# Kernel optimization log

Measured on AMD Instinct MI355X. Metric: run time of the kernel, lower is better.

Reference implementation:

```python
import jax, jax.numpy as jnp
import numpy as np

INPLANES = 768
HIDDEN = 64
NUM_EXPERTS = 6
TOP_K = 2


def setup_inputs() -> dict:
    key = jax.random.key(0)
    ks = jax.random.split(key, 7)
    B, C, D = 64, 320, INPLANES
    x = jax.random.normal(ks[0], (B, C, D), dtype=jnp.float32)
    xi = jax.random.normal(ks[1], (B, C, D), dtype=jnp.float32)
    # gating network: per-token logits over experts
    w_gate = jax.random.normal(ks[2], (D, NUM_EXPERTS), dtype=jnp.float32) / np.sqrt(D)
    # LoRA-style experts: down-projection D -> HIDDEN per expert
    expert_w = jax.random.normal(ks[3], (NUM_EXPERTS, D, HIDDEN), dtype=jnp.float32) / np.sqrt(D)
    expert_b = jnp.zeros((NUM_EXPERTS, HIDDEN), dtype=jnp.float32)
    # reprojection ffn1_1: Linear(HIDDEN, INPLANES), torch convention W:[out,in]
    ffn1_w = jax.random.normal(ks[4], (D, HIDDEN), dtype=jnp.float32) / np.sqrt(HIDDEN)
    ffn1_b = jnp.zeros((D,), dtype=jnp.float32)
    return {"x": x, "xi": xi, "w_gate": w_gate, "expert_w": expert_w,
            "expert_b": expert_b, "ffn1_w": ffn1_w, "ffn1_b": ffn1_b}


def _cv_squared(v):
    eps = 1e-10
    return jnp.var(v) / (jnp.mean(v) ** 2 + eps)


def reference(x, xi, w_gate, expert_w, expert_b, ffn1_w, ffn1_b):
    B, C, D = x.shape
    nz = C // 5
    # slice template (z) and search (x) token streams from both modalities
    z0, x0 = x[:, :nz, :], x[:, nz:, :]
    z1, x1 = xi[:, :nz, :], xi[:, nz:, :]
    # MoE_lora: fuse the two modalities and route tokens (z tokens first, then x)
    inp = jnp.concatenate([z0 + z1, x0 + x1], axis=1)        # [B, C, D]
    tok = inp.reshape(-1, D)                                  # [N, D], N = B*C
    N = tok.shape[0]
    # noisy-top-k gating (clean/eval path): top-2 experts, softmax over kept logits
    logits = tok @ w_gate                                     # [N, E]
    top_vals, top_idx = jax.lax.top_k(logits, TOP_K)          # [N, k]
    top_gates = jax.nn.softmax(top_vals, axis=-1)             # [N, k]
    gates = jnp.zeros_like(logits).at[jnp.arange(N)[:, None], top_idx].add(top_gates)
    # expert LoRA down-projections, combined by sparse gates (dense-equivalent math)
    h = jnp.einsum('nd,edh->enh', tok, expert_w) + expert_b[:, None, :]  # [E, N, H]
    y = jnp.einsum('ne,enh->nh', gates, h)                    # [N, H]
    y = y.reshape(B, C, HIDDEN)
    z_moe, x_moe = y[:, :nz, :], y[:, nz:, :]
    # load-balancing loss: cv^2 of importance + cv^2 of load
    importance = gates.sum(axis=0)
    load = (gates > 0).astype(jnp.float32).sum(axis=0)
    loss = _cv_squared(importance) + _cv_squared(load)
    # ffn1_1 reprojection back to inplanes
    x_prompted = x_moe @ ffn1_w.T + ffn1_b                    # [B, 4C/5, D]
    z_prompted = z_moe @ ffn1_w.T + ffn1_b                    # [B, C/5, D]
    return (x_prompted, z_prompted, loss, logits)
```

## Files before the change

kernel.cpp:

```cpp
#include <hip/hip_runtime.h>

typedef __attribute__((ext_vector_type(8))) short short8;
typedef __attribute__((ext_vector_type(4))) short short4v;
typedef __attribute__((ext_vector_type(4))) float f32x4;

#define VM(n) asm volatile("s_waitcnt vmcnt(" #n ")" ::: "memory")
#define LGKM0 asm volatile("s_waitcnt lgkmcnt(0)" ::: "memory")

namespace {

constexpr int DIN  = 768;
constexpr int HID  = 64;
constexpr int NEXP = 6;
constexpr int CDIM  = 320;
constexpr int NZ    = 64;
constexpr int NTOK  = 20480;

constexpr long long XP_OFF   = 0;
constexpr long long ZP_OFF   = 12582912LL;
constexpr long long LOSS_OFF = 15728640LL;
constexpr long long LG_OFF   = 15728641LL;

__device__ inline unsigned short f2bf(float f) {
  union { float f; unsigned u; } v{f};
  return (unsigned short)((v.u + 0x7FFFu + ((v.u >> 16) & 1u)) >> 16);
}
__device__ inline float b2f(unsigned short s) {
  union { unsigned u; float f; } v{(unsigned)s << 16};
  return v.f;
}
__device__ inline void gload16(const void* g, void* l) {
  __builtin_amdgcn_global_load_lds(
      (const __attribute__((address_space(1))) unsigned*)g,
      (__attribute__((address_space(3))) unsigned*)l, 16, 0, 0);
}
__device__ inline int row_base(int n) {
  int bb = n / CDIM, c = n - bb * CDIM;
  return (c < NZ) ? (int)(ZP_OFF + (long long)(bb * NZ + c) * DIN)
                  : (int)(XP_OFF + (long long)(bb * (CDIM - NZ) + (c - NZ)) * DIN);
}

__global__ __launch_bounds__(512) void pre_kernel(
    const float* __restrict__ x, const float* __restrict__ xi,
    const float* __restrict__ wg, const float* __restrict__ ew,
    const float* __restrict__ fw,
    float* __restrict__ out, float4* __restrict__ rec,
    unsigned short* __restrict__ ewb_t, unsigned short* __restrict__ fwb)
{
  int b = blockIdx.x, tid = threadIdx.x;
  __shared__ __align__(16) char sbuf[67584];
  if (b < 72) {
    float (*t_lds)[65] = (float(*)[65])sbuf;
    int e = b / 12, kc = (b % 12) * 64;
    const float* src = ew + (size_t)e * DIN * HID + (size_t)kc * HID;
    #pragma unroll
    for (int it = 0; it < 8; ++it) {
      int f = it * 512 + tid; int ky = f >> 6, h = f & 63;
      t_lds[h][ky] = src[ky * 64 + h];
    }
    __syncthreads();
    unsigned short* dst = ewb_t + (size_t)e * DIN * HID + kc;
    #pragma unroll
    for (int it = 0; it < 8; ++it) {
      int f = it * 512 + tid; int h = f >> 6, ky = f & 63;
      dst[(size_t)h * DIN + ky] = f2bf(t_lds[h][ky]);
    }
    return;
  }
  if (b < 84) {
    int base = (b - 72) * 4096;
    #pragma unroll
    for (int it = 0; it < 8; ++it) {
      int idx = base + it * 512 + tid;
      fwb[idx] = f2bf(fw[idx]);
    }
    return;
  }
  char* xl = sbuf;
  char* il = sbuf + 24576;
  const float* wgl = (const float*)(sbuf + 49152);
  int t0 = (b - 84) * 8;

  #pragma unroll
  for (int it = 0; it < 3; ++it) {
    int s = it * 512 + tid;
    gload16(x  + (size_t)t0 * DIN + s * 4, xl + s * 16);
    gload16(xi + (size_t)t0 * DIN + s * 4, il + s * 16);
  }
  #pragma unroll
  for (int it = 0; it < 3; ++it) {
    int s = it * 512 + tid;
    if (s < NEXP * DIN / 4) gload16(wg + s * 4, sbuf + 49152 + s * 16);
  }
  VM(0);
  __builtin_amdgcn_s_barrier();

  int lane = tid & 63, w = tid >> 6;
  int n = t0 + w;
  unsigned short* tk = (unsigned short*)out + (size_t)row_base(n) * 2;

  float lg[NEXP];
  #pragma unroll
  for (int e = 0; e < NEXP; ++e) lg[e] = 0.f;

  #pragma unroll
  for (int j = 0; j < 3; ++j) {
    int d = lane * 4 + 256 * j;
    float4 a = *(const float4*)(xl + w * 3072 + d * 4);
    float4 q = *(const float4*)(il + w * 3072 + d * 4);
    float tv0 = a.x + q.x, tv1 = a.y + q.y, tv2 = a.z + q.z, tv3 = a.w + q.w;
    short4v t4;
    t4[0] = (short)f2bf(tv0); t4[1] = (short)f2bf(tv1);
    t4[2] = (short)f2bf(tv2); t4[3] = (short)f2bf(tv3);
    *(short4v*)(tk + d) = t4;
    const float4* wq = (const float4*)(wgl + d * 6);
    float4 w0 = wq[0], w1 = wq[1], w2 = wq[2], w3 = wq[3], w4 = wq[4], w5 = wq[5];
    lg[0] += tv0 * w0.x; lg[1] += tv0 * w0.y; lg[2] += tv0 * w0.z;
    lg[3] += tv0 * w0.w; lg[4] += tv0 * w1.x; lg[5] += tv0 * w1.y;
    lg[0] += tv1 * w1.z; lg[1] += tv1 * w1.w; lg[2] += tv1 * w2.x;
    lg[3] += tv1 * w2.y; lg[4] += tv1 * w2.z; lg[5] += tv1 * w2.w;
    lg[0] += tv2 * w3.x; lg[1] += tv2 * w3.y; lg[2] += tv2 * w3.z;
    lg[3] += tv2 * w3.w; lg[4] += tv2 * w4.x; lg[5] += tv2 * w4.y;
    lg[0] += tv3 * w4.z; lg[1] += tv3 * w4.w; lg[2] += tv3 * w5.x;
    lg[3] += tv3 * w5.y; lg[4] += tv3 * w5.z; lg[5] += tv3 * w5.w;
  }
  #pragma unroll
  for (int e = 0; e < NEXP; ++e) {
    float v = lg[e];
    #pragma unroll
    for (int off = 32; off >= 1; off >>= 1) v += __shfl_xor(v, off, 64);
    lg[e] = v;
  }
  int e0 = 0; float v0 = lg[0];
  #pragma unroll
  for (int j = 1; j < NEXP; ++j) if (lg[j] > v0) { v0 = lg[j]; e0 = j; }
  int e1 = 0; float v1 = -3.4e38f;
  #pragma unroll
  for (int j = 0; j < NEXP; ++j) if (j != e0 && lg[j] > v1) { v1 = lg[j]; e1 = j; }
  float g0 = 1.f / (1.f + expf(v1 - v0));
  if (lane < NEXP) {
    float myv = lg[0];
    #pragma unroll
    for (int e = 1; e < NEXP; ++e) if (lane == e) myv = lg[e];
    out[LG_OFF + (size_t)n * NEXP + lane] = myv;
  }
  if (lane == 0) rec[n] = make_float4((float)e0, (float)e1, g0, 1.f - g0);
}

__global__ __launch_bounds__(512) void moe_kernel(
    const unsigned short* __restrict__ ewb_t, const float* __restrict__ eb,
    const unsigned short* __restrict__ fwb, const float* __restrict__ fb,
    const float4* __restrict__ rec, float* __restrict__ out)
{
  __shared__ __align__(16) char smem[74752];
  __shared__ int rb[64];
  __shared__ float simp[8][NEXP], sld[8][NEXP];

  int tid = threadIdx.x, lane = tid & 63, wid = tid >> 6;
  int qw = lane >> 4, l15 = lane & 15;
  int wm = wid >> 2, wn = wid & 3;

  if (blockIdx.x == 320) {
    float imp[NEXP], ld[NEXP];
    #pragma unroll
    for (int e = 0; e < NEXP; ++e) { imp[e] = 0.f; ld[e] = 0.f; }
    for (int n = tid; n < NTOK; n += 512) {
      float4 r = rec[n];
      int e0 = (int)r.x, e1 = (int)r.y;
      #pragma unroll
      for (int e = 0; e < NEXP; ++e) {
        imp[e] += (e == e0 ? r.z : 0.f) + (e == e1 ? r.w : 0.f);
        ld[e]  += (e == e0 ? 1.f : 0.f) + (e == e1 ? 1.f : 0.f);
      }
    }
    #pragma unroll
    for (int e = 0; e < NEXP; ++e) {
      float a = imp[e], bq = ld[e];
      #pragma unroll
      for (int off = 32; off >= 1; off >>= 1) {
        a += __shfl_xor(a, off, 64);
        bq += __shfl_xor(bq, off, 64);
      }
      imp[e] = a; ld[e] = bq;
    }
    if (lane == 0) {
      #pragma unroll
      for (int e = 0; e < NEXP; ++e) { simp[wid][e] = imp[e]; sld[wid][e] = ld[e]; }
    }
    __syncthreads();
    if (tid == 0) {
      float It[NEXP], Lt[NEXP], mi = 0.f, ml = 0.f;
      #pragma unroll
      for (int e = 0; e < NEXP; ++e) {
        It[e] = 0.f; Lt[e] = 0.f;
        #pragma unroll
        for (int w = 0; w < 8; ++w) { It[e] += simp[w][e]; Lt[e] += sld[w][e]; }
        mi += It[e]; ml += Lt[e];
      }
      mi /= NEXP; ml /= NEXP;
      float vi = 0.f, vl = 0.f;
      #pragma unroll
      for (int e = 0; e < NEXP; ++e) {
        vi += (It[e] - mi) * (It[e] - mi);
        vl += (Lt[e] - ml) * (Lt[e] - ml);
      }
      vi /= NEXP; vl /= NEXP;
      out[LOSS_OFF] = vi / (mi * mi + 1e-10f) + vl / (ml * ml + 1e-10f);
    }
    return;
  }

  int t0 = blockIdx.x * 64;
  const unsigned short* tokb = (const unsigned short*)out;

  size_t b_src[3]; int b_dst[3];
  #pragma unroll
  for (int it = 0; it < 3; ++it) {
    int F = it * 512 + tid, r = F >> 2, s = F & 3;
    b_src[it] = (size_t)r * DIN + ((s ^ (r & 3) ^ ((r & 4) >> 1)) << 3);
    b_dst[it] = (it * 512 + wid * 64) * 16;
  }
  int ar = tid >> 2, as = tid & 3;
  size_t a_src = (size_t)row_base(t0 + ar) * 2 +
                 ((as ^ (ar & 3) ^ ((ar & 4) >> 1)) << 3);
  int a_dst = (wid * 64) * 16;

  if (tid < 64) rb[tid] = row_base(t0 + tid);

  #pragma unroll
  for (int it = 0; it < 3; ++it)
    gload16(ewb_t + b_src[it], smem + 8192 + b_dst[it]);
  if (tid < 256) gload16(tokb + a_src, smem + a_dst);

  f32x4 acc[2][6];
  #pragma unroll
  for (int m = 0; m < 2; ++m)
    #pragma unroll
    for (int n = 0; n < 6; ++n) acc[m][n] = (f32x4){0.f, 0.f, 0.f, 0.f};

  int aoff[2], boff[6];
  #pragma unroll
  for (int m = 0; m < 2; ++m) {
    int row = wm * 32 + m * 16 + l15;
    aoff[m] = row * 64 + ((qw ^ (row & 3) ^ ((row & 4) >> 1)) << 4);
  }
  #pragma unroll
  for (int n = 0; n < 6; ++n) {
    int row = wn * 96 + n * 16 + l15;
    boff[n] = row * 64 + ((qw ^ (row & 3) ^ ((row & 4) >> 1)) << 4);
  }

  for (int k = 0; k < 24; ++k) {
    const char* cA = smem + (k & 1) * 4096;
    const char* cB = smem + 8192 + (k & 1) * 24576;
    char* nA = (char*)smem + ((k + 1) & 1) * 4096;
    char* nB = (char*)smem + 8192 + ((k + 1) & 1) * 24576;
    if (k < 23) {
      #pragma unroll
      for (int it = 0; it < 3; ++it)
        gload16(ewb_t + b_src[it] + (k + 1) * 32, nB + b_dst[it]);
      if (tid < 256) gload16(tokb + a_src + (k + 1) * 32, nA + a_dst);
      if (wid < 4) VM(4); else VM(3);
    } else {
      VM(0);
    }
    __builtin_amdgcn_s_barrier();
    __builtin_amdgcn_sched_barrier(0);
    short8 af[2], bfv[6];
    #pragma unroll
    for (int m = 0; m < 2; ++m) af[m] = *(const short8*)(cA + aoff[m]);
    #pragma unroll
    for (int n = 0; n < 6; ++n) bfv[n] = *(const short8*)(cB + boff[n]);
    __builtin_amdgcn_s_setprio(1);
    #pragma unroll
    for (int m = 0; m < 2; ++m)
      #pragma unroll
      for (int n = 0; n < 6; ++n)
        acc[m][n] = __builtin_amdgcn_mfma_f32_16x16x32_bf16(af[m], bfv[n], acc[m][n], 0, 0, 0);
    __builtin_amdgcn_s_setprio(0);
    __builtin_amdgcn_sched_barrier(0);
    __builtin_amdgcn_s_barrier();
  }

  #pragma unroll
  for (int it = 0; it < 2; ++it) {
    int F = it * 512 + tid, r = F >> 3, s = F & 7;
    gload16(fwb + (size_t)r * HID + ((s ^ (r & 7)) << 3),
            smem + 58368 + (it * 512 + wid * 64) * 16);
  }

  unsigned short* hl = (unsigned short*)(smem + 8192);
  #pragma unroll
  for (int m = 0; m < 2; ++m)
    #pragma unroll
    for (int n = 0; n < 6; ++n)
      #pragma unroll
      for (int i = 0; i < 4; ++i) {
        int row = wm * 32 + m * 16 + qw * 4 + i;
        int col = wn * 96 + n * 16 + l15;
        hl[row * 392 + col] = f2bf(acc[m][n][i]);
      }
  LGKM0;
  __builtin_amdgcn_s_barrier();

  {
    int t = tid >> 3, j0 = (tid & 7) * 8;
    float4 rr = rec[t0 + t];
    int e0 = (int)rr.x, e1 = (int)rr.y;
    float g0 = rr.z, g1 = rr.w;
    short8 h0 = *(const short8*)(hl + t * 392 + e0 * 64 + j0);
    short8 h1 = *(const short8*)(hl + t * 392 + e1 * 64 + j0);
    const float4* ep0 = (const float4*)(eb + e0 * 64 + j0);
    const float4* ep1 = (const float4*)(eb + e1 * 64 + j0);
    float4 b0a = ep0[0], b0b = ep0[1], b1a = ep1[0], b1b = ep1[1];
    float be0[8] = {b0a.x, b0a.y, b0a.z, b0a.w, b0b.x, b0b.y, b0b.z, b0b.w};
    float be1[8] = {b1a.x, b1a.y, b1a.z, b1a.w, b1b.x, b1b.y, b1b.z, b1b.w};
    short8 ov;
    #pragma unroll
    for (int j = 0; j < 8; ++j) {
      float v = g0 * (b2f((unsigned short)h0[j]) + be0[j])
              + g1 * (b2f((unsigned short)h1[j]) + be1[j]);
      ov[j] = (short)f2bf(v);
    }
    *(short8*)(smem + t * 128 + ((((tid & 7)) ^ (t & 7)) << 4)) = ov;
  }
  LGKM0;
  __builtin_amdgcn_s_barrier();

  for (int c = 0; c < 6; ++c) {
    const char* cF = smem + ((c & 1) ? 8192 : 58368);
    char* nF = (char*)smem + ((c & 1) ? 58368 : 8192);
    if (c < 5) {
      #pragma unroll
      for (int it = 0; it < 2; ++it) {
        int F = it * 512 + tid, r = F >> 3, s = F & 7;
        gload16(fwb + (size_t)((c + 1) * 128 + r) * HID + ((s ^ (r & 7)) << 3),
                nF + (it * 512 + wid * 64) * 16);
      }
      VM(2);
    } else {
      VM(0);
    }
    __builtin_amdgcn_s_barrier();
    __builtin_amdgcn_sched_barrier(0);
    f32x4 a2[2][2];
    #pragma unroll
    for (int m = 0; m < 2; ++m)
      #pragma unroll
      for (int n = 0; n < 2; ++n) a2[m][n] = (f32x4){0.f, 0.f, 0.f, 0.f};
    #pragma unroll
    for (int kk = 0; kk < 2; ++kk) {
      short8 ay[2], bw[2];
      #pragma unroll
      for (int m = 0; m < 2; ++m) {
        int row = wm * 32 + m * 16 + l15;
        ay[m] = *(const short8*)(smem + row * 128 + (((kk * 4 + qw) ^ (row & 7)) << 4));
      }
      #pragma unroll
      for (int n = 0; n < 2; ++n) {
        int rw = wn * 32 + n * 16 + l15;
        bw[n] = *(const short8*)(cF + rw * 128 + (((kk * 4 + qw) ^ (rw & 7)) << 4));
      }
      __builtin_amdgcn_s_setprio(1);
      #pragma unroll
      for (int m = 0; m < 2; ++m)
        #pragma unroll
        for (int n = 0; n < 2; ++n)
          a2[m][n] = __builtin_amdgcn_mfma_f32_16x16x32_bf16(ay[m], bw[n], a2[m][n], 0, 0, 0);
      __builtin_amdgcn_s_setprio(0);
    }
    #pragma unroll
    for (int n = 0; n < 2; ++n) {
      int col = c * 128 + wn * 32 + n * 16 + l15;
      float bias = fb[col];
      #pragma unroll
      for (int m = 0; m < 2; ++m)
        #pragma unroll
        for (int i = 0; i < 4; ++i) {
          int rl = wm * 32 + m * 16 + qw * 4 + i;
          out[(size_t)rb[rl] + col] = a2[m][n][i] + bias;
        }
    }
    __builtin_amdgcn_sched_barrier(0);
    __builtin_amdgcn_s_barrier();
  }
}

}

extern "C" void kernel_launch(void* const* d_in, const int* in_sizes, int n_in,
                              void* d_out, int out_size, void* d_ws, size_t ws_size,
                              hipStream_t stream)
{
  const float* x  = (const float*)d_in[0];
  const float* xi = (const float*)d_in[1];
  const float* wg = (const float*)d_in[2];
  const float* ew = (const float*)d_in[3];
  const float* eb = (const float*)d_in[4];
  const float* fw = (const float*)d_in[5];
  const float* fb = (const float*)d_in[6];
  float* out = (float*)d_out;

  char* w = (char*)d_ws;
  float4*         rec   = (float4*)w;
  unsigned short* ewb_t = (unsigned short*)(w + 327680);
  unsigned short* fwb   = (unsigned short*)(w + 327680 + 589824);

  pre_kernel<<<84 + 2560, 512, 0, stream>>>(x, xi, wg, ew, fw, out, rec, ewb_t, fwb);
  moe_kernel<<<321, 512, 0, stream>>>(ewb_t, eb, fwb, fb, rec, out);
}
```

Measured before the change: 68.65 us.

## Make gating pre-kernel persistent with double-buffered async token loads

The gating/cast part of pre_kernel now has each block handle 80 tokens in 10 steps of 8, with two LDS buffers. The global-to-LDS load for step s+2 is issued while step s is computed, and the gate weights are loaded and transposed into LDS once per block. The grid drops from 2560 to 256 gating blocks, which cuts per-block launch and weight-load overhead. The larger 114 KB LDS footprint allows only one block per CU and fewer blocks than before, so overall parallelism and memory-level parallelism may fall.

```diff
diff --git a/kernel.cpp b/kernel.cpp
--- a/kernel.cpp
+++ b/kernel.cpp
@@ -48,7 +48,7 @@
     unsigned short* __restrict__ ewb_t, unsigned short* __restrict__ fwb)
 {
   int b = blockIdx.x, tid = threadIdx.x;
-  __shared__ __align__(16) char sbuf[67584];
+  __shared__ __align__(16) char sbuf[116736];
   if (b < 72) {
     float (*t_lds)[65] = (float(*)[65])sbuf;
     int e = b / 12, kc = (b % 12) * 64;
@@ -76,75 +76,108 @@
     }
     return;
   }
-  char* xl = sbuf;
-  char* il = sbuf + 24576;
-  const float* wgl = (const float*)(sbuf + 49152);
-  int t0 = (b - 84) * 8;
+  float* wgt = (float*)sbuf;
+  char*  buf0 = sbuf + 18432;
+  char*  buf1 = sbuf + 67584;
+  int t0 = (b - 84) * 80;
+  int lane = tid & 63, w = tid >> 6;
 
   #pragma unroll
   for (int it = 0; it < 3; ++it) {
     int s = it * 512 + tid;
-    gload16(x  + (size_t)t0 * DIN + s * 4, xl + s * 16);
-    gload16(xi + (size_t)t0 * DIN + s * 4, il + s * 16);
-  }
+    if (s < NEXP * DIN / 4) gload16(wg + s * 4, buf0 + s * 16);
+  }
+  VM(0);
+  __builtin_amdgcn_s_barrier();
+  {
+    const float* lin = (const float*)buf0;
+    #pragma unroll
+    for (int i = 0; i < 9; ++i) {
+      int idx = i * 512 + tid;
+      int d = idx / 6, e = idx - 6 * d;
+      wgt[e * DIN + d] = lin[idx];
+    }
+  }
+  LGKM0;
+  __builtin_amdgcn_s_barrier();
+
   #pragma unroll
   for (int it = 0; it < 3; ++it) {
     int s = it * 512 + tid;
-    if (s < NEXP * DIN / 4) gload16(wg + s * 4, sbuf + 49152 + s * 16);
-  }
-  VM(0);
-  __builtin_amdgcn_s_barrier();
-
-  int lane = tid & 63, w = tid >> 6;
-  int n = t0 + w;
-  unsigned short* tk = (unsigned short*)out + (size_t)row_base(n) * 2;
-
-  float lg[NEXP];
-  #pragma unroll
-  for (int e = 0; e < NEXP; ++e) lg[e] = 0.f;
-
-  #pragma unroll
-  for (int j = 0; j < 3; ++j) {
-    int d = lane * 4 + 256 * j;
-    float4 a = *(const float4*)(xl + w * 3072 + d * 4);
-    float4 q = *(const float4*)(il + w * 3072 + d * 4);
-    float tv0 = a.x + q.x, tv1 = a.y + q.y, tv2 = a.z + q.z, tv3 = a.w + q.w;
-    short4v t4;
-    t4[0] = (short)f2bf(tv0); t4[1] = (short)f2bf(tv1);
-    t4[2] = (short)f2bf(tv2); t4[3] = (short)f2bf(tv3);
-    *(short4v*)(tk + d) = t4;
-    const float4* wq = (const float4*)(wgl + d * 6);
-    float4 w0 = wq[0], w1 = wq[1], w2 = wq[2], w3 = wq[3], w4 = wq[4], w5 = wq[5];
-    lg[0] += tv0 * w0.x; lg[1] += tv0 * w0.y; lg[2] += tv0 * w0.z;
-    lg[3] += tv0 * w0.w; lg[4] += tv0 * w1.x; lg[5] += tv0 * w1.y;
-    lg[0] += tv1 * w1.z; lg[1] += tv1 * w1.w; lg[2] += tv1 * w2.x;
-    lg[3] += tv1 * w2.y; lg[4] += tv1 * w2.z; lg[5] += tv1 * w2.w;
-    lg[0] += tv2 * w3.x; lg[1] += tv2 * w3.y; lg[2] += tv2 * w3.z;
-    lg[3] += tv2 * w3.w; lg[4] += tv2 * w4.x; lg[5] += tv2 * w4.y;
-    lg[0] += tv3 * w4.z; lg[1] += tv3 * w4.w; lg[2] += tv3 * w5.x;
-    lg[3] += tv3 * w5.y; lg[4] += tv3 * w5.z; lg[5] += tv3 * w5.w;
-  }
-  #pragma unroll
-  for (int e = 0; e < NEXP; ++e) {
-    float v = lg[e];
-    #pragma unroll
-    for (int off = 32; off >= 1; off >>= 1) v += __shfl_xor(v, off, 64);
-    lg[e] = v;
-  }
-  int e0 = 0; float v0 = lg[0];
-  #pragma unroll
-  for (int j = 1; j < NEXP; ++j) if (lg[j] > v0) { v0 = lg[j]; e0 = j; }
-  int e1 = 0; float v1 = -3.4e38f;
-  #pragma unroll
-  for (int j = 0; j < NEXP; ++j) if (j != e0 && lg[j] > v1) { v1 = lg[j]; e1 = j; }
-  float g0 = 1.f / (1.f + expf(v1 - v0));
-  if (lane < NEXP) {
-    float myv = lg[0];
-    #pragma unroll
-    for (int e = 1; e < NEXP; ++e) if (lane == e) myv = lg[e];
-    out[LG_OFF + (size_t)n * NEXP + lane] = myv;
-  }
-  if (lane == 0) rec[n] = make_float4((float)e0, (float)e1, g0, 1.f - g0);
+    gload16(x  + (size_t)t0 * DIN + s * 4, buf0 + s * 16);
+    gload16(xi + (size_t)t0 * DIN + s * 4, buf0 + 24576 + s * 16);
+  }
+  #pragma unroll
+  for (int it = 0; it < 3; ++it) {
+    int s = it * 512 + tid;
+    gload16(x  + (size_t)(t0 + 8) * DIN + s * 4, buf1 + s * 16);
+    gload16(xi + (size_t)(t0 + 8) * DIN + s * 4, buf1 + 24576 + s * 16);
+  }
+
+  for (int s = 0; s < 10; ++s) {
+    char* cbuf = (s & 1) ? buf1 : buf0;
+    if (s < 9) { VM(6); } else { VM(0); }
+    __builtin_amdgcn_s_barrier();
+    __builtin_amdgcn_sched_barrier(0);
+
+    int n = t0 + s * 8 + w;
+    unsigned short* tk = (unsigned short*)out + (size_t)row_base(n) * 2;
+    const char* xl = cbuf;
+    const char* il = cbuf + 24576;
+
+    float lg[NEXP];
+    #pragma unroll
+    for (int e = 0; e < NEXP; ++e) lg[e] = 0.f;
+
+    #pragma unroll
+    for (int j = 0; j < 3; ++j) {
+      int d = lane * 4 + 256 * j;
+      float4 a = *(const float4*)(xl + w * 3072 + d * 4);
+      float4 q = *(const float4*)(il + w * 3072 + d * 4);
+      float tv0 = a.x + q.x, tv1 = a.y + q.y, tv2 = a.z + q.z, tv3 = a.w + q.w;
+      short4v t4;
+      t4[0] = (short)f2bf(tv0); t4[1] = (short)f2bf(tv1);
+      t4[2] = (short)f2bf(tv2); t4[3] = (short)f2bf(tv3);
+      *(short4v*)(tk + d) = t4;
+      #pragma unroll
+      for (int e = 0; e < NEXP; ++e) {
+        float4 wv = *(const float4*)(wgt + e * DIN + d);
+        lg[e] += tv0 * wv.x + tv1 * wv.y + tv2 * wv.z + tv3 * wv.w;
+      }
+    }
+    #pragma unroll
+    for (int e = 0; e < NEXP; ++e) {
+      float v = lg[e];
+      #pragma unroll
+      for (int off = 32; off >= 1; off >>= 1) v += __shfl_xor(v, off, 64);
+      lg[e] = v;
+    }
+    int e0 = 0; float v0 = lg[0];
+    #pragma unroll
+    for (int j = 1; j < NEXP; ++j) if (lg[j] > v0) { v0 = lg[j]; e0 = j; }
+    int e1 = 0; float v1 = -3.4e38f;
+    #pragma unroll
+    for (int j = 0; j < NEXP; ++j) if (j != e0 && lg[j] > v1) { v1 = lg[j]; e1 = j; }
+    float g0 = 1.f / (1.f + expf(v1 - v0));
+    if (lane < NEXP) {
+      float myv = lg[0];
+      #pragma unroll
+      for (int e = 1; e < NEXP; ++e) if (lane == e) myv = lg[e];
+      out[LG_OFF + (size_t)n * NEXP + lane] = myv;
+    }
+    if (lane == 0) rec[n] = make_float4((float)e0, (float)e1, g0, 1.f - g0);
+
+    LGKM0;
+    __builtin_amdgcn_s_barrier();
+    if (s + 2 < 10) {
+      #pragma unroll
+      for (int it = 0; it < 3; ++it) {
+        int si = it * 512 + tid;
+        gload16(x  + (size_t)(t0 + (s + 2) * 8) * DIN + si * 4, cbuf + si * 16);
+        gload16(xi + (size_t)(t0 + (s + 2) * 8) * DIN + si * 4, cbuf + 24576 + si * 16);
+      }
+    }
+  }
 }
 
 __global__ __launch_bounds__(512) void moe_kernel(
@@ -406,6 +439,6 @@
   unsigned short* ewb_t = (unsigned short*)(w + 327680);
   unsigned short* fwb   = (unsigned short*)(w + 327680 + 589824);
 
-  pre_kernel<<<84 + 2560, 512, 0, stream>>>(x, xi, wg, ew, fw, out, rec, ewb_t, fwb);
+  pre_kernel<<<84 + 256, 512, 0, stream>>>(x, xi, wg, ew, fw, out, rec, ewb_t, fwb);
   moe_kernel<<<321, 512, 0, stream>>>(ewb_t, eb, fwb, fb, rec, out);
 }
```

After: 72.17 us. 1.05x slower.
